# Kernel tuning notes

Measured on AMD Instinct MI355X. Metric: run time of the kernel, lower is better.

## Reference

```python
import jax, jax.numpy as jnp
import numpy as np
from jax import lax

COCO_80_TO_91 = [1,2,3,4,5,6,7,8,9,10,11,13,14,15,16,17,18,19,20,21,22,23,24,25,27,28,31,32,33,34,35,36,37,38,39,40,41,42,43,44,46,47,48,49,50,51,52,53,54,55,56,57,58,59,60,61,62,63,64,65,67,70,72,73,74,75,76,77,78,79,80,81,82,84,85,86,87,88,89,90]

CONF = 0.25      # self.confidence
IOU_THR = 0.7    # ultralytics NMS default
TOPK = 1000      # candidate cap before NMS
MAX_DET = 300    # ultralytics max_det default
MAX_WH = 7680.0  # per-class offset trick
IMG_SZ = 640.0   # yolov8 letterboxed input size


def setup_inputs() -> dict:
    key = jax.random.key(0)
    preds = jax.random.uniform(key, (32, 84, 8400), dtype=jnp.float32)
    return {"preds": preds}


def _nms_single(boxes, scores):
    """Greedy NMS on score-descending boxes [K,4] (class-offset xyxy). Returns keep mask [K]."""
    K = boxes.shape[0]
    area = (boxes[:, 2] - boxes[:, 0]) * (boxes[:, 3] - boxes[:, 1])  # [K]
    lt = jnp.maximum(boxes[:, None, :2], boxes[None, :, :2])          # [K,K,2]
    rb = jnp.minimum(boxes[:, None, 2:], boxes[None, :, 2:])
    wh = jnp.clip(rb - lt, 0.0)
    inter = wh[..., 0] * wh[..., 1]
    iou = inter / (area[:, None] + area[None, :] - inter + 1e-7)       # [K,K]
    idx = jnp.arange(K)
    sup = (iou > IOU_THR) & (idx[None, :] > idx[:, None])              # i suppresses later j

    def body(i, keep):
        return jnp.where(keep[i], keep & ~sup[i], keep)

    return lax.fori_loop(0, K, body, jnp.ones((K,), dtype=bool))


def reference(preds):
    # preds: [B, 84, N] -> [B, N, 84]
    p = jnp.transpose(preds, (0, 2, 1))
    box_xywh = p[..., :4] * IMG_SZ           # xywh in pixels on 640x640 canvas
    cls = p[..., 4:]                          # [B, N, 80]
    scores = jnp.max(cls, axis=-1)            # best-class confidence
    labels = jnp.argmax(cls, axis=-1)         # 0..79
    xy, wh = box_xywh[..., :2], box_xywh[..., 2:]
    xyxy = jnp.concatenate([xy - wh * 0.5, xy + wh * 0.5], axis=-1)  # decode

    # confidence filter + top-K candidate selection (score-descending)
    s_masked = jnp.where(scores > CONF, scores, -1.0)
    top_s, top_i = lax.top_k(s_masked, TOPK)                          # [B,TOPK]
    top_b = jnp.take_along_axis(xyxy, top_i[..., None], axis=1)      # [B,TOPK,4]
    top_l = jnp.take_along_axis(labels, top_i, axis=1)               # [B,TOPK]

    # per-class NMS via class offset
    off_b = top_b + (top_l.astype(top_b.dtype) * MAX_WH)[..., None]
    keep = jax.vmap(_nms_single)(off_b, top_s) & (top_s > CONF)

    # select final max_det detections, zero-pad invalid slots
    fin_s = jnp.where(keep, top_s, -1.0)
    out_s, out_i = lax.top_k(fin_s, MAX_DET)                          # [B,MAX_DET]
    out_b = jnp.take_along_axis(top_b, out_i[..., None], axis=1)
    out_l = jnp.take_along_axis(top_l, out_i, axis=1)
    valid = out_s > CONF
    boxes = jnp.where(valid[..., None], out_b, 0.0)
    scores_out = jnp.where(valid, out_s, 0.0)
    mapped = jnp.asarray(COCO_80_TO_91, dtype=jnp.int64)[out_l]       # COCO 80 -> 91 ids
    labels_out = jnp.where(valid, mapped, 0)
    return boxes, scores_out, labels_out
```

## Files before the change

### kernel.cpp

```cpp
#include <hip/hip_runtime.h>
#include <stdint.h>

typedef unsigned long long u64;
typedef unsigned int u32;

#define BATCH 32
#define NCH 84
#define NA 8400
#define NCLS 80
#define TOPK 1000
#define MAXDET 300
#define CONF 0.25f
#define IOU_T 0.7f
#define MAX_WH 7680.0f
#define IMG_SZ 640.0f
#define NT 1024
#define KPT 9
#define NCOPY 8
#define HPAD 260
#define DTILE 256

__device__ __constant__ float coco_map_f[NCLS] = {
    1,2,3,4,5,6,7,8,9,10,11,13,14,15,16,17,18,19,20,21,22,23,24,25,27,28,
    31,32,33,34,35,36,37,38,39,40,41,42,43,44,46,47,48,49,50,51,52,53,54,
    55,56,57,58,59,60,61,62,63,64,65,67,70,72,73,74,75,76,77,78,79,80,81,
    82,84,85,86,87,88,89,90};

__device__ inline u64 shflx64(u64 v, int m) {
    int lo = __shfl_xor((int)(u32)(v & 0xFFFFFFFFull), m, 64);
    int hi = __shfl_xor((int)(u32)(v >> 32), m, 64);
    return ((u64)(u32)hi << 32) | (u32)lo;
}

__global__ __launch_bounds__(256)
void decode_kernel(const float* __restrict__ preds,
                   u64* __restrict__ keys,
                   float4* __restrict__ boxes,
                   int* __restrict__ labels) {
    const int b = blockIdx.y;
    const int a_base = blockIdx.x * DTILE;
    const int t = threadIdx.x;
    const int a = a_base + t;
    const float* p = preds + (size_t)b * NCH * NA;

    __shared__ float stage[16][DTILE];

    float bx = 0.f, by = 0.f, bw = 0.f, bh = 0.f;
    float best = -1.0f;
    int bl = 0;

    for (int chunk = 0; chunk < 6; ++chunk) {
        const int r0 = chunk * 16;
        const int nr = (chunk == 5) ? 4 : 16;
        if (chunk) __syncthreads();
        for (int i = 0; i < nr / 4; ++i) {
            int idx = i * 256 + t;
            int rl = idx >> 6;
            int c4 = (idx & 63) * 4;
            int col = a_base + c4;
            float4 v = (col < NA) ? *(const float4*)(p + (size_t)(r0 + rl) * NA + col)
                                  : make_float4(0.f, 0.f, 0.f, 0.f);
            *(float4*)&stage[rl][c4] = v;
        }
        __syncthreads();
        if (chunk == 0) {
            bx = stage[0][t]; by = stage[1][t];
            bw = stage[2][t]; bh = stage[3][t];
            best = stage[4][t]; bl = 0;
            for (int r = 5; r < 16; ++r) {
                float v = stage[r][t];
                int c = r - 4;
                bl = (v > best) ? c : bl;  best = fmaxf(v, best);
            }
        } else {
            for (int r = 0; r < nr; ++r) {
                float v = stage[r][t];
                int c = r0 + r - 4;
                bl = (v > best) ? c : bl;  best = fmaxf(v, best);
            }
        }
    }

    if (a < NA) {
        float fx = bx * IMG_SZ, fy = by * IMG_SZ;
        float fw = bw * IMG_SZ, fh = bh * IMG_SZ;
        float hw = fw * 0.5f, hh = fh * 0.5f;
        boxes[(size_t)b * NA + a] = make_float4(fx - hw, fy - hh, fx + hw, fy + hh);
        float s = (best > CONF) ? best : -1.0f;
        u32 fb = __float_as_uint(s);
        u32 u = (fb & 0x80000000u) ? ~fb : (fb | 0x80000000u);
        keys[(size_t)b * NA + a] = ((u64)u << 14) | (u64)(16383 - a);
        labels[(size_t)b * NA + a] = bl;
    }
}

__global__ __launch_bounds__(NT)
void select_nms_kernel(const u64* __restrict__ keys,
                       const float4* __restrict__ boxes,
                       const int* __restrict__ labels,
                       float* __restrict__ out) {
    const int b = blockIdx.x;
    const int t = threadIdx.x;
    const int lane = t & 63, wid = t >> 6;

    __shared__ union {
        struct {
            u64 sk[2][NT];
            int hist[NCOPY * HPAD];
        } a;
        struct {
            float offb[TOPK][4];
            float area[TOPK];
            u64 cmask2[NCLS][16];
            unsigned short rows[NCLS][64];
        } bb;
    } u_s;
    __shared__ unsigned char lb8[TOPK];
    __shared__ unsigned char keep[TOPK];
    __shared__ int selB, selK, hselS, smax, scnt, cnt, ktot_s;
    __shared__ int wsum[16], woff[16];

    u64 kreg[KPT];
    const u64* kb = keys + (size_t)b * NA;
    int nk = 0;
    for (int i = t; i < NA; i += NT) kreg[nk++] = kb[i];

    u64 P = 0ull;
    int kk = TOPK;
    int nsel = 0;
    for (int d = 5; d >= 0; --d) {
        __syncthreads();
        if (t == 0) { smax = -1; scnt = 0; }
        __syncthreads();
        u64 hmask = (~0ull) << (8 * (d + 1));
        int dig[KPT];
        int mymax = -1;
#pragma unroll
        for (int i = 0; i < KPT; ++i) {
            bool act = (i < nk) && (((kreg[i] ^ P) & hmask) == 0ull);
            dig[i] = act ? (int)((kreg[i] >> (8 * d)) & 255) : -1;
            mymax = max(mymax, dig[i]);
        }
#pragma unroll
        for (int off = 32; off; off >>= 1)
            mymax = max(mymax, __shfl_down(mymax, off, 64));
        if (lane == 0) atomicMax(&smax, mymax);
        __syncthreads();
        int maxb = smax;
        int myc = 0;
#pragma unroll
        for (int i = 0; i < KPT; ++i) myc += (dig[i] == maxb) ? 1 : 0;
#pragma unroll
        for (int off = 32; off; off >>= 1) myc += __shfl_down(myc, off, 64);
        if (lane == 0) atomicAdd(&scnt, myc);
        __syncthreads();
        int cm = scnt;
        if (cm >= kk) {
            P |= ((u64)maxb) << (8 * d);
            nsel = TOPK - kk + cm;
            if (nsel <= NT) break;
            continue;
        }
        for (int i = t; i < NCOPY * HPAD; i += NT) u_s.a.hist[i] = 0;
        __syncthreads();
        int* myh = u_s.a.hist + (wid & (NCOPY - 1)) * HPAD;
#pragma unroll
        for (int i = 0; i < KPT; ++i)
            if (dig[i] >= 0) atomicAdd(&myh[dig[i]], 1);
        __syncthreads();
        if (t < 64) {
            int h0 = 0, h1 = 0, h2 = 0, h3 = 0;
            for (int c = 0; c < NCOPY; ++c) {
                const int* hp = u_s.a.hist + c * HPAD + 4 * t;
                h0 += hp[0]; h1 += hp[1]; h2 += hp[2]; h3 += hp[3];
            }
            int s = h0 + h1 + h2 + h3;
            int S = s;
            #pragma unroll
            for (int off = 1; off < 64; off <<= 1) {
                int o = __shfl_down(S, off, 64);
                if (t + off < 64) S += o;
            }
            int Snext = S - s;
            int c3 = Snext + h3, c2 = c3 + h2, c1 = c2 + h1, c0 = c1 + h0;
            int cand = -1, above = 0;
            if (c0 >= kk) {
                if      (c3 >= kk) { cand = 4 * t + 3; above = Snext; }
                else if (c2 >= kk) { cand = 4 * t + 2; above = c3; }
                else if (c1 >= kk) { cand = 4 * t + 1; above = c2; }
                else               { cand = 4 * t;     above = c1; }
            }
            int pc = (cand < 0) ? 0 : (((cand + 1) << 16) | (kk - above));
            #pragma unroll
            for (int off = 32; off; off >>= 1)
                pc = max(pc, __shfl_down(pc, off, 64));
            pc = __shfl(pc, 0, 64);
            int B = (pc >> 16) - 1;
            if (t == (B >> 2)) {
                int m4 = B & 3;
                selB = B;
                selK = pc & 0xFFFF;
                hselS = (m4 == 0) ? h0 : (m4 == 1) ? h1 : (m4 == 2) ? h2 : h3;
            }
        }
        __syncthreads();
        P |= ((u64)selB) << (8 * d);
        kk = selK;
        nsel = TOPK - kk + hselS;
        if (nsel <= NT) break;
    }

    __syncthreads();
    if (t == 0) cnt = 0;
    __syncthreads();
    for (int i = 0; i < KPT; ++i) {
        bool p = (i < nk) && (kreg[i] >= P);
        u64 m = __ballot(p);
        int base = 0;
        if (lane == 0) base = atomicAdd(&cnt, (int)__popcll(m));
        base = __shfl(base, 0, 64);
        if (p) u_s.a.sk[0][base + (int)__popcll(m & ((1ull << lane) - 1ull))] = kreg[i];
    }
    if (t < NT - nsel) u_s.a.sk[0][nsel + t] = 0ull;
    __syncthreads();

    u64 myk = u_s.a.sk[0][t];
    int buf = 1;
    for (int size = 2; size <= NT; size <<= 1) {
        bool up = ((t & size) == 0);
        for (int stride = size >> 1; stride; stride >>= 1) {
            u64 pk;
            if (stride >= 64) {
                u_s.a.sk[buf][t] = myk;
                __syncthreads();
                pk = u_s.a.sk[buf][t ^ stride];
                buf ^= 1;
            } else {
                pk = shflx64(myk, stride);
            }
            bool tlow = ((t & stride) == 0);
            u64 mn = (myk < pk) ? myk : pk;
            u64 mx = (myk < pk) ? pk : myk;
            myk = up ? (tlow ? mx : mn) : (tlow ? mn : mx);
        }
    }

    __syncthreads();
    for (int i = t; i < NCLS * 16; i += NT) ((u64*)u_s.bb.cmask2)[i] = 0ull;
    __syncthreads();

    int my_a = -1, my_L = 0;
    if (t < TOPK) {
        my_a = 16383 - (int)(myk & 16383ull);
        my_L = labels[(size_t)b * NA + my_a];
        lb8[t] = (unsigned char)my_L;
        float4 bx = boxes[(size_t)b * NA + my_a];
        float off = (float)my_L * MAX_WH;
        float ox0 = bx.x + off, oy0 = bx.y + off, ox1 = bx.z + off, oy1 = bx.w + off;
        u_s.bb.offb[t][0] = ox0; u_s.bb.offb[t][1] = oy0;
        u_s.bb.offb[t][2] = ox1; u_s.bb.offb[t][3] = oy1;
        u_s.bb.area[t] = (ox1 - ox0) * (oy1 - oy0);
        keep[t] = 1;
        atomicOr(&u_s.bb.cmask2[my_L][t >> 6], 1ull << (t & 63));
    }
    __syncthreads();

    for (int c = wid; c < NCLS; c += 16) {
        u64 w = (lane < 16) ? u_s.bb.cmask2[c][lane] : 0ull;
        int cw = __popcll(w);
        int pre = cw;
        #pragma unroll
        for (int off = 1; off < 16; off <<= 1) {
            int o = __shfl_up(pre, off, 64);
            if (lane >= off) pre += o;
        }
        int n = __shfl(pre, 15, 64);
        pre -= cw;
        if (n == 0) continue;
        if (n <= 64) {
            if (lane < 16) {
                u64 ww = w; int base = pre, boff = lane << 6;
                while (ww) {
                    int bit = __ffsll((long long)ww) - 1;
                    ww &= ww - 1;
                    u_s.bb.rows[c][base++] = (unsigned short)(boff + bit);
                }
            }
            int j = (lane < n) ? (int)u_s.bb.rows[c][lane] : (int)u_s.bb.rows[c][0];
            float x0 = u_s.bb.offb[j][0], y0 = u_s.bb.offb[j][1];
            float x1 = u_s.bb.offb[j][2], y1 = u_s.bb.offb[j][3];
            float ar = u_s.bb.area[j];
            u64 colm = 0ull;
            for (int i = 0; i < n; ++i) {
                float hx0 = __shfl(x0, i, 64);
                float hy0 = __shfl(y0, i, 64);
                float hx1 = __shfl(x1, i, 64);
                float hy1 = __shfl(y1, i, 64);
                float ha  = __shfl(ar, i, 64);
                float lx = fmaxf(hx0, x0), ly = fmaxf(hy0, y0);
                float rx = fminf(hx1, x1), ry = fminf(hy1, y1);
                float ww2 = fmaxf(rx - lx, 0.0f);
                float hh2 = fmaxf(ry - ly, 0.0f);
                float inter = ww2 * hh2;
                float denom = ha + ar;
                denom = denom - inter;
                denom = denom + 1e-7f;
                bool s = (lane > i) && (lane < n) && (inter / denom > IOU_T);
                colm |= ((u64)s) << i;
            }
            u64 alive = (n >= 64) ? ~0ull : ((1ull << n) - 1ull);
            for (int i = 0; i < n; ++i) {
                if (!((alive >> i) & 1ull)) continue;
                alive &= ~__ballot((colm >> i) & 1ull);
            }
            if (lane < n) keep[j] = (unsigned char)((alive >> lane) & 1ull);
        } else if (lane == 0) {
            for (int i = 0; i < TOPK; ++i) {
                if (lb8[i] != (unsigned char)c || !keep[i]) continue;
                float ax0 = u_s.bb.offb[i][0], ay0 = u_s.bb.offb[i][1];
                float ax1 = u_s.bb.offb[i][2], ay1 = u_s.bb.offb[i][3];
                float aa = u_s.bb.area[i];
                for (int j2 = i + 1; j2 < TOPK; ++j2) {
                    if (lb8[j2] != (unsigned char)c || !keep[j2]) continue;
                    float lx = fmaxf(ax0, u_s.bb.offb[j2][0]);
                    float ly = fmaxf(ay0, u_s.bb.offb[j2][1]);
                    float rx = fminf(ax1, u_s.bb.offb[j2][2]);
                    float ry = fminf(ay1, u_s.bb.offb[j2][3]);
                    float ww2 = fmaxf(rx - lx, 0.0f);
                    float hh2 = fmaxf(ry - ly, 0.0f);
                    float inter = ww2 * hh2;
                    float denom = aa + u_s.bb.area[j2];
                    denom = denom - inter;
                    denom = denom + 1e-7f;
                    if (inter / denom > IOU_T) keep[j2] = 0;
                }
            }
        }
    }
    __syncthreads();

    bool valid = false;
    float sj = 0.0f;
    if (t < TOPK) {
        u32 u = (u32)(myk >> 14);
        u32 fb = (u & 0x80000000u) ? (u ^ 0x80000000u) : ~u;
        sj = __uint_as_float(fb);
        valid = keep[t] && (sj > CONF);
    }
    u64 m = __ballot(valid);
    if (lane == 0) wsum[wid] = (int)__popcll(m);
    __syncthreads();
    if (wid == 0) {
        int v = (lane < 16) ? wsum[lane] : 0;
        #pragma unroll
        for (int off = 1; off < 16; off <<= 1) {
            int o = __shfl_up(v, off, 64);
            if (lane >= off) v += o;
        }
        if (lane < 16) woff[lane] = v - wsum[lane];
        if (lane == 15) ktot_s = v;
    }
    __syncthreads();
    int ktot = ktot_s;
    int rank = woff[wid] + (int)__popcll(m & ((1ull << lane) - 1ull));

    float* out_boxes = out;
    float* out_scores = out + (size_t)BATCH * MAXDET * 4;
    float* out_labels = out + (size_t)BATCH * MAXDET * 5;
    if (valid && rank < MAXDET) {
        float4 bx = boxes[(size_t)b * NA + my_a];
        float* ob = out_boxes + ((size_t)b * MAXDET + rank) * 4;
        ob[0] = bx.x; ob[1] = bx.y; ob[2] = bx.z; ob[3] = bx.w;
        out_scores[(size_t)b * MAXDET + rank] = sj;
        out_labels[(size_t)b * MAXDET + rank] = coco_map_f[my_L];
    }
    if (t < MAXDET && t >= ktot) {
        float* ob = out_boxes + ((size_t)b * MAXDET + t) * 4;
        ob[0] = 0.0f; ob[1] = 0.0f; ob[2] = 0.0f; ob[3] = 0.0f;
        out_scores[(size_t)b * MAXDET + t] = 0.0f;
        out_labels[(size_t)b * MAXDET + t] = 0.0f;
    }
}

extern "C" void kernel_launch(void* const* d_in, const int* in_sizes, int n_in,
                              void* d_out, int out_size, void* d_ws, size_t ws_size,
                              hipStream_t stream) {
    const float* preds = (const float*)d_in[0];
    char* ws = (char*)d_ws;

    const size_t keys_bytes  = (size_t)BATCH * NA * 8;
    const size_t boxes_bytes = (size_t)BATCH * NA * 16;

    u64* keys = (u64*)ws;
    float4* boxes = (float4*)(ws + keys_bytes);
    int* labels = (int*)(ws + keys_bytes + boxes_bytes);
    float* out = (float*)d_out;

    dim3 dgrid((NA + DTILE - 1) / DTILE, BATCH);
    decode_kernel<<<dgrid, 256, 0, stream>>>(preds, keys, boxes, labels);
    select_nms_kernel<<<BATCH, NT, 0, stream>>>(keys, boxes, labels, out);
}
```

Baseline: 184.4 us.

## Split select+NMS into separate kernels with per-class NMS blocks across grid

Splits the fused per-batch select/sort/NMS kernel into three kernels. The sort kernel writes the sorted keys, gathered boxes and per-class compacted candidate lists to global memory. A new NMS kernel launches one 64-thread block per (class, batch), so the 80 classes of each image run on separate CUs instead of being serialized over 16 wavefronts of one block. An epilogue kernel then compacts and writes the outputs. This spreads NMS over many more CUs, at the cost of two extra launches and global round-trips for the intermediate arrays.

```diff
diff --git a/kernel.cpp b/kernel.cpp
--- a/kernel.cpp
+++ b/kernel.cpp
@@ -95,10 +95,18 @@
 }
 
 __global__ __launch_bounds__(NT)
-void select_nms_kernel(const u64* __restrict__ keys,
-                       const float4* __restrict__ boxes,
-                       const int* __restrict__ labels,
-                       float* __restrict__ out) {
+void select_sort_kernel(const u64* __restrict__ keys,
+                        const float4* __restrict__ boxes,
+                        const int* __restrict__ labels,
+                        u64* __restrict__ sortedk,
+                        float4* __restrict__ gbox,
+                        float4* __restrict__ goffr,
+                        float* __restrict__ garear,
+                        unsigned char* __restrict__ lbr,
+                        float4* __restrict__ goffb,
+                        float* __restrict__ garea,
+                        unsigned short* __restrict__ grank,
+                        int* __restrict__ gccnt) {
     const int b = blockIdx.x;
     const int t = threadIdx.x;
     const int lane = t & 63, wid = t >> 6;
@@ -109,16 +117,10 @@
             int hist[NCOPY * HPAD];
         } a;
         struct {
-            float offb[TOPK][4];
-            float area[TOPK];
             u64 cmask2[NCLS][16];
-            unsigned short rows[NCLS][64];
         } bb;
     } u_s;
-    __shared__ unsigned char lb8[TOPK];
-    __shared__ unsigned char keep[TOPK];
-    __shared__ int selB, selK, hselS, smax, scnt, cnt, ktot_s;
-    __shared__ int wsum[16], woff[16];
+    __shared__ int selB, selK, hselS, smax, scnt, cnt;
 
     u64 kreg[KPT];
     const u64* kb = keys + (size_t)b * NA;
@@ -244,108 +246,141 @@
             myk = up ? (tlow ? mx : mn) : (tlow ? mn : mx);
         }
     }
+    sortedk[(size_t)b * NT + t] = myk;
 
     __syncthreads();
     for (int i = t; i < NCLS * 16; i += NT) ((u64*)u_s.bb.cmask2)[i] = 0ull;
     __syncthreads();
 
-    int my_a = -1, my_L = 0;
+    int my_L = 0;
+    float4 bx = make_float4(0.f, 0.f, 0.f, 0.f);
+    float ox0 = 0.f, oy0 = 0.f, ox1 = 0.f, oy1 = 0.f, ar = 0.f;
     if (t < TOPK) {
-        my_a = 16383 - (int)(myk & 16383ull);
+        int my_a = 16383 - (int)(myk & 16383ull);
         my_L = labels[(size_t)b * NA + my_a];
-        lb8[t] = (unsigned char)my_L;
-        float4 bx = boxes[(size_t)b * NA + my_a];
+        bx = boxes[(size_t)b * NA + my_a];
         float off = (float)my_L * MAX_WH;
-        float ox0 = bx.x + off, oy0 = bx.y + off, ox1 = bx.z + off, oy1 = bx.w + off;
-        u_s.bb.offb[t][0] = ox0; u_s.bb.offb[t][1] = oy0;
-        u_s.bb.offb[t][2] = ox1; u_s.bb.offb[t][3] = oy1;
-        u_s.bb.area[t] = (ox1 - ox0) * (oy1 - oy0);
-        keep[t] = 1;
+        ox0 = bx.x + off; oy0 = bx.y + off; ox1 = bx.z + off; oy1 = bx.w + off;
+        ar = (ox1 - ox0) * (oy1 - oy0);
         atomicOr(&u_s.bb.cmask2[my_L][t >> 6], 1ull << (t & 63));
     }
     __syncthreads();
-
-    for (int c = wid; c < NCLS; c += 16) {
-        u64 w = (lane < 16) ? u_s.bb.cmask2[c][lane] : 0ull;
-        int cw = __popcll(w);
-        int pre = cw;
-        #pragma unroll
-        for (int off = 1; off < 16; off <<= 1) {
-            int o = __shfl_up(pre, off, 64);
-            if (lane >= off) pre += o;
-        }
-        int n = __shfl(pre, 15, 64);
-        pre -= cw;
-        if (n == 0) continue;
-        if (n <= 64) {
-            if (lane < 16) {
-                u64 ww = w; int base = pre, boff = lane << 6;
-                while (ww) {
-                    int bit = __ffsll((long long)ww) - 1;
-                    ww &= ww - 1;
-                    u_s.bb.rows[c][base++] = (unsigned short)(boff + bit);
-                }
-            }
-            int j = (lane < n) ? (int)u_s.bb.rows[c][lane] : (int)u_s.bb.rows[c][0];
-            float x0 = u_s.bb.offb[j][0], y0 = u_s.bb.offb[j][1];
-            float x1 = u_s.bb.offb[j][2], y1 = u_s.bb.offb[j][3];
-            float ar = u_s.bb.area[j];
-            u64 colm = 0ull;
-            for (int i = 0; i < n; ++i) {
-                float hx0 = __shfl(x0, i, 64);
-                float hy0 = __shfl(y0, i, 64);
-                float hx1 = __shfl(x1, i, 64);
-                float hy1 = __shfl(y1, i, 64);
-                float ha  = __shfl(ar, i, 64);
-                float lx = fmaxf(hx0, x0), ly = fmaxf(hy0, y0);
-                float rx = fminf(hx1, x1), ry = fminf(hy1, y1);
-                float ww2 = fmaxf(rx - lx, 0.0f);
-                float hh2 = fmaxf(ry - ly, 0.0f);
-                float inter = ww2 * hh2;
-                float denom = ha + ar;
+    if (t < TOPK) {
+        int w = t >> 6;
+        int r = __popcll(u_s.bb.cmask2[my_L][w] & ((1ull << (t & 63)) - 1ull));
+        for (int q = 0; q < w; ++q) r += __popcll(u_s.bb.cmask2[my_L][q]);
+        gbox[(size_t)b * NT + t] = bx;
+        goffr[(size_t)b * NT + t] = make_float4(ox0, oy0, ox1, oy1);
+        garear[(size_t)b * NT + t] = ar;
+        lbr[(size_t)b * NT + t] = (unsigned char)my_L;
+        if (r < 64) {
+            size_t ci = ((size_t)b * NCLS + my_L) * 64 + r;
+            goffb[ci] = make_float4(ox0, oy0, ox1, oy1);
+            garea[ci] = ar;
+            grank[ci] = (unsigned short)t;
+        }
+    }
+    if (t < NCLS) {
+        int s = 0;
+#pragma unroll
+        for (int q = 0; q < 16; ++q) s += __popcll(u_s.bb.cmask2[t][q]);
+        gccnt[(size_t)b * NCLS + t] = s;
+    }
+}
+
+__global__ __launch_bounds__(64)
+void nms_kernel(const float4* __restrict__ goffb,
+                const float* __restrict__ garea,
+                const unsigned short* __restrict__ grank,
+                const int* __restrict__ gccnt,
+                const float4* __restrict__ goffr,
+                const float* __restrict__ garear,
+                const unsigned char* __restrict__ lbr,
+                unsigned char* __restrict__ keepg) {
+    const int c = blockIdx.x;
+    const int b = blockIdx.y;
+    const int lane = threadIdx.x;
+    const int n = gccnt[(size_t)b * NCLS + c];
+    if (n == 0) return;
+
+    if (n <= 64) {
+        size_t ci = ((size_t)b * NCLS + c) * 64 + lane;
+        float4 bb = make_float4(0.f, 0.f, 0.f, 0.f);
+        float ar = 0.f;
+        int rk = 0;
+        if (lane < n) { bb = goffb[ci]; ar = garea[ci]; rk = grank[ci]; }
+        u64 colm = 0ull;
+        for (int i = 0; i < n; ++i) {
+            float hx0 = __shfl(bb.x, i, 64);
+            float hy0 = __shfl(bb.y, i, 64);
+            float hx1 = __shfl(bb.z, i, 64);
+            float hy1 = __shfl(bb.w, i, 64);
+            float ha  = __shfl(ar, i, 64);
+            float lx = fmaxf(hx0, bb.x), ly = fmaxf(hy0, bb.y);
+            float rx = fminf(hx1, bb.z), ry = fminf(hy1, bb.w);
+            float w = fmaxf(rx - lx, 0.0f);
+            float h = fmaxf(ry - ly, 0.0f);
+            float inter = w * h;
+            float denom = ha + ar;
+            denom = denom - inter;
+            denom = denom + 1e-7f;
+            bool s = (lane > i) && (lane < n) && (inter / denom > IOU_T);
+            colm |= ((u64)s) << i;
+        }
+        u64 alive = (n >= 64) ? ~0ull : ((1ull << n) - 1ull);
+        for (int i = 0; i < n; ++i) {
+            if (!((alive >> i) & 1ull)) continue;
+            alive &= ~__ballot((colm >> i) & 1ull);
+        }
+        if (lane < n) keepg[(size_t)b * NT + rk] = (unsigned char)((alive >> lane) & 1ull);
+    } else if (lane == 0) {
+        u64 aliveW[16];
+        for (int q = 0; q < 16; ++q) aliveW[q] = ~0ull;
+        for (int i = 0; i < TOPK; ++i) {
+            if (lbr[(size_t)b * NT + i] != (unsigned char)c) continue;
+            if (!((aliveW[i >> 6] >> (i & 63)) & 1ull)) continue;
+            float4 bi = goffr[(size_t)b * NT + i];
+            float ai = garear[(size_t)b * NT + i];
+            for (int j = i + 1; j < TOPK; ++j) {
+                if (lbr[(size_t)b * NT + j] != (unsigned char)c) continue;
+                if (!((aliveW[j >> 6] >> (j & 63)) & 1ull)) continue;
+                float4 bj = goffr[(size_t)b * NT + j];
+                float lx = fmaxf(bi.x, bj.x), ly = fmaxf(bi.y, bj.y);
+                float rx = fminf(bi.z, bj.z), ry = fminf(bi.w, bj.w);
+                float w = fmaxf(rx - lx, 0.0f);
+                float h = fmaxf(ry - ly, 0.0f);
+                float inter = w * h;
+                float denom = ai + garear[(size_t)b * NT + j];
                 denom = denom - inter;
                 denom = denom + 1e-7f;
-                bool s = (lane > i) && (lane < n) && (inter / denom > IOU_T);
-                colm |= ((u64)s) << i;
-            }
-            u64 alive = (n >= 64) ? ~0ull : ((1ull << n) - 1ull);
-            for (int i = 0; i < n; ++i) {
-                if (!((alive >> i) & 1ull)) continue;
-                alive &= ~__ballot((colm >> i) & 1ull);
-            }
-            if (lane < n) keep[j] = (unsigned char)((alive >> lane) & 1ull);
-        } else if (lane == 0) {
-            for (int i = 0; i < TOPK; ++i) {
-                if (lb8[i] != (unsigned char)c || !keep[i]) continue;
-                float ax0 = u_s.bb.offb[i][0], ay0 = u_s.bb.offb[i][1];
-                float ax1 = u_s.bb.offb[i][2], ay1 = u_s.bb.offb[i][3];
-                float aa = u_s.bb.area[i];
-                for (int j2 = i + 1; j2 < TOPK; ++j2) {
-                    if (lb8[j2] != (unsigned char)c || !keep[j2]) continue;
-                    float lx = fmaxf(ax0, u_s.bb.offb[j2][0]);
-                    float ly = fmaxf(ay0, u_s.bb.offb[j2][1]);
-                    float rx = fminf(ax1, u_s.bb.offb[j2][2]);
-                    float ry = fminf(ay1, u_s.bb.offb[j2][3]);
-                    float ww2 = fmaxf(rx - lx, 0.0f);
-                    float hh2 = fmaxf(ry - ly, 0.0f);
-                    float inter = ww2 * hh2;
-                    float denom = aa + u_s.bb.area[j2];
-                    denom = denom - inter;
-                    denom = denom + 1e-7f;
-                    if (inter / denom > IOU_T) keep[j2] = 0;
-                }
-            }
-        }
-    }
-    __syncthreads();
-
+                if (inter / denom > IOU_T) aliveW[j >> 6] &= ~(1ull << (j & 63));
+            }
+        }
+        for (int i = 0; i < TOPK; ++i)
+            if (lbr[(size_t)b * NT + i] == (unsigned char)c)
+                keepg[(size_t)b * NT + i] = (unsigned char)((aliveW[i >> 6] >> (i & 63)) & 1ull);
+    }
+}
+
+__global__ __launch_bounds__(NT)
+void epilogue_kernel(const u64* __restrict__ sortedk,
+                     const unsigned char* __restrict__ keepg,
+                     const float4* __restrict__ gbox,
+                     const unsigned char* __restrict__ lbr,
+                     float* __restrict__ out) {
+    const int b = blockIdx.x;
+    const int t = threadIdx.x;
+    const int lane = t & 63, wid = t >> 6;
+    __shared__ int wsum[16], woff[16], ktot_s;
+
+    u64 myk = sortedk[(size_t)b * NT + t];
     bool valid = false;
     float sj = 0.0f;
     if (t < TOPK) {
         u32 u = (u32)(myk >> 14);
         u32 fb = (u & 0x80000000u) ? (u ^ 0x80000000u) : ~u;
         sj = __uint_as_float(fb);
-        valid = keep[t] && (sj > CONF);
+        valid = keepg[(size_t)b * NT + t] && (sj > CONF);
     }
     u64 m = __ballot(valid);
     if (lane == 0) wsum[wid] = (int)__popcll(m);
@@ -368,11 +403,11 @@
     float* out_scores = out + (size_t)BATCH * MAXDET * 4;
     float* out_labels = out + (size_t)BATCH * MAXDET * 5;
     if (valid && rank < MAXDET) {
-        float4 bx = boxes[(size_t)b * NA + my_a];
+        float4 bx = gbox[(size_t)b * NT + t];
         float* ob = out_boxes + ((size_t)b * MAXDET + rank) * 4;
         ob[0] = bx.x; ob[1] = bx.y; ob[2] = bx.z; ob[3] = bx.w;
         out_scores[(size_t)b * MAXDET + rank] = sj;
-        out_labels[(size_t)b * MAXDET + rank] = coco_map_f[my_L];
+        out_labels[(size_t)b * MAXDET + rank] = coco_map_f[lbr[(size_t)b * NT + t]];
     }
     if (t < MAXDET && t >= ktot) {
         float* ob = out_boxes + ((size_t)b * MAXDET + t) * 4;
@@ -387,16 +422,31 @@
                               hipStream_t stream) {
     const float* preds = (const float*)d_in[0];
     char* ws = (char*)d_ws;
-
-    const size_t keys_bytes  = (size_t)BATCH * NA * 8;
-    const size_t boxes_bytes = (size_t)BATCH * NA * 16;
-
-    u64* keys = (u64*)ws;
-    float4* boxes = (float4*)(ws + keys_bytes);
-    int* labels = (int*)(ws + keys_bytes + boxes_bytes);
+    size_t off = 0;
+    auto alloc = [&](size_t bytes) { char* p = ws + off; off += (bytes + 255) & ~(size_t)255; return p; };
+
+    u64* keys            = (u64*)           alloc((size_t)BATCH * NA * 8);
+    float4* boxes        = (float4*)        alloc((size_t)BATCH * NA * 16);
+    int* labels          = (int*)           alloc((size_t)BATCH * NA * 4);
+    u64* sortedk         = (u64*)           alloc((size_t)BATCH * NT * 8);
+    float4* gbox         = (float4*)        alloc((size_t)BATCH * NT * 16);
+    float4* goffr        = (float4*)        alloc((size_t)BATCH * NT * 16);
+    float* garear        = (float*)         alloc((size_t)BATCH * NT * 4);
+    unsigned char* lbr   = (unsigned char*) alloc((size_t)BATCH * NT);
+    float4* goffb        = (float4*)        alloc((size_t)BATCH * NCLS * 64 * 16);
+    float* garea         = (float*)         alloc((size_t)BATCH * NCLS * 64 * 4);
+    unsigned short* grank= (unsigned short*)alloc((size_t)BATCH * NCLS * 64 * 2);
+    int* gccnt           = (int*)           alloc((size_t)BATCH * NCLS * 4);
+    unsigned char* keepg = (unsigned char*) alloc((size_t)BATCH * NT);
     float* out = (float*)d_out;
 
     dim3 dgrid((NA + DTILE - 1) / DTILE, BATCH);
     decode_kernel<<<dgrid, 256, 0, stream>>>(preds, keys, boxes, labels);
-    select_nms_kernel<<<BATCH, NT, 0, stream>>>(keys, boxes, labels, out);
-}
+    select_sort_kernel<<<BATCH, NT, 0, stream>>>(keys, boxes, labels, sortedk,
+                                                 gbox, goffr, garear, lbr,
+                                                 goffb, garea, grank, gccnt);
+    dim3 ngrid(NCLS, BATCH);
+    nms_kernel<<<ngrid, 64, 0, stream>>>(goffb, garea, grank, gccnt,
+                                         goffr, garear, lbr, keepg);
+    epilogue_kernel<<<BATCH, NT, 0, stream>>>(sortedk, keepg, gbox, lbr, out);
+}
```

After: 174.2 us. 5.5% less time.
